# Kernel tuning notes

Hardware: AMD Instinct MI355X
Metric: run time of the kernel (lower is better)

The kernel has to match this reference:

```python
import jax, jax.numpy as jnp
import numpy as np

OLD_CL = 16
RATIO = 1.0
IGNORE_INDEX = 255


def setup_inputs() -> dict:
    key = jax.random.key(0)
    k1, k2 = jax.random.split(key)
    N, C, H, W = 8, 21, 512, 512
    inputs = jax.random.normal(k1, (N, C, H, W), dtype=jnp.float32)
    targets = jax.random.randint(k2, (N, H, W), 0, C).astype(jnp.int32)
    return {"inputs": inputs, "targets": targets}


def _forward(inputs, targets):
    N, C, H, W = inputs.shape
    # unbiased log-prob remap: old classes collapsed into channel 0
    den = jax.nn.logsumexp(inputs, axis=1)                       # [N,H,W]
    out0 = jax.nn.logsumexp(inputs[:, :OLD_CL], axis=1) - den    # [N,H,W]
    outputs = jnp.zeros_like(inputs)                             # channels 1..OLD_CL-1 stay 0
    outputs = outputs.at[:, 0].set(out0)
    outputs = outputs.at[:, OLD_CL:].set(inputs[:, OLD_CL:] - den[:, None])

    labels = jnp.where(targets < OLD_CL, 0, targets)             # [N,H,W]

    # per-sample class histogram (device-side replacement for the per-sample
    # cpu torch.histc loop). histc(bins=C, min=0, max=C-1) on integer-valued
    # labels counts occurrences per class, dropping values outside [0, C-1].
    lab_flat = labels.reshape(N, -1)
    in_range = lab_flat < C
    seg = jnp.where(in_range, lab_flat, 0) + jnp.arange(N, dtype=lab_flat.dtype)[:, None] * C
    hist = jax.ops.segment_sum(
        in_range.astype(jnp.float32).reshape(-1), seg.reshape(-1), num_segments=N * C
    ).reshape(N, C)

    cls = jnp.arange(C)
    idx_old = (cls < OLD_CL) & (cls != 0)                        # [C], old classes except 0
    idx0 = hist == 0                                             # computed on raw hist
    hist = hist.at[:, 0].set(hist[:, :OLD_CL].sum(axis=1))
    hist = jnp.where(idx_old[None, :], 0.0, hist)
    hist = jnp.where(idx0 & ~idx_old[None, :], 1.0, hist)
    weight = jnp.power(hist.sum(axis=1, keepdims=True) / hist, RATIO)
    weight = jnp.where(idx_old[None, :], 0.0, weight)            # kills the infs from /0
    weight = jax.lax.stop_gradient(weight)                       # torch .detach()

    outputs = outputs * weight[:, :, None, None]

    # nll_loss with ignore_index, mean reduction over valid pixels
    valid = labels != IGNORE_INDEX
    safe = jnp.where(valid, labels, 0)
    picked = jnp.take_along_axis(outputs, safe[:, None], axis=1)[:, 0]  # [N,H,W]
    vmask = valid.astype(outputs.dtype)
    return -(picked * vmask).sum() / vmask.sum()


def reference(inputs, targets):
    return _forward(inputs, targets)
```

## Files before the change

kernel.cpp:

```cpp
#include <hip/hip_runtime.h>

#define NS 8
#define NC 21
#define HW (512*512)
#define OLD 16
#define LBLK 128
#define LITER 2
#define PSTRIDE 16


__global__ void __launch_bounds__(256) loss_hist_kernel(const float* __restrict__ in,
                                                        const int* __restrict__ tgt,
                                                        float* __restrict__ part) {
    int n   = blockIdx.x >> 7;
    int blk = blockIdx.x & (LBLK - 1);
    const float* inN = in + (size_t)n * (NC * HW);
    const int4*  t4  = reinterpret_cast<const int4*>(tgt + (size_t)n * HW);

    float s[6]   = {0.f, 0.f, 0.f, 0.f, 0.f, 0.f};
    int   cnt[6] = {0, 0, 0, 0, 0, 0};

#pragma unroll 1
    for (int it = 0; it < LITER; ++it) {
        int g = (blk * LITER + it) * 256 + threadIdx.x;
        int p = g * 4;
        int4 t = t4[g];

        float4 sa  = make_float4(0.f, 0.f, 0.f, 0.f);
        float4 s16 = make_float4(0.f, 0.f, 0.f, 0.f);
        float4 xl  = make_float4(0.f, 0.f, 0.f, 0.f);

#pragma unroll
        for (int c = 0; c < NC; ++c) {
            float4 x = *reinterpret_cast<const float4*>(inN + (size_t)c * HW + p);
            sa.x += __expf(x.x);
            sa.y += __expf(x.y);
            sa.z += __expf(x.z);
            sa.w += __expf(x.w);
            if (c == OLD - 1) s16 = sa;
            if (c >= OLD) {
                xl.x = (t.x == c) ? x.x : xl.x;
                xl.y = (t.y == c) ? x.y : xl.y;
                xl.z = (t.z == c) ? x.z : xl.z;
                xl.w = (t.w == c) ? x.w : xl.w;
            }
        }

        int   labs[4] = {t.x, t.y, t.z, t.w};
        float sal[4]  = {sa.x, sa.y, sa.z, sa.w};
        float s16l[4] = {s16.x, s16.y, s16.z, s16.w};
        float xll[4]  = {xl.x, xl.y, xl.z, xl.w};
#pragma unroll
        for (int j = 0; j < 4; ++j) {
            int lab = labs[j] < OLD ? 0 : labs[j];
            float den = __logf(sal[j]);
            float val = (lab == 0 ? __logf(s16l[j]) : xll[j]) - den;

            bool h0 = (lab == 0);
            s[0]  += h0 ? val : 0.0f;  cnt[0] += h0;
#pragma unroll
            for (int k = 1; k < 6; ++k) {
                bool hk = (lab == 15 + k);
                s[k]  += hk ? val : 0.0f;
                cnt[k] += hk;
            }
        }
    }

#pragma unroll
    for (int off = 32; off > 0; off >>= 1)
#pragma unroll
        for (int k = 0; k < 6; ++k) {
            s[k]   += __shfl_down(s[k], off, 64);
            cnt[k] += __shfl_down(cnt[k], off, 64);
        }

    __shared__ float sp[4][6];
    __shared__ int   sc[4][6];
    int wave = threadIdx.x >> 6;
    if ((threadIdx.x & 63) == 0)
#pragma unroll
        for (int k = 0; k < 6; ++k) { sp[wave][k] = s[k]; sc[wave][k] = cnt[k]; }
    __syncthreads();
    if (threadIdx.x < 6) {
        int k = threadIdx.x;
        float fs = sp[0][k] + sp[1][k] + sp[2][k] + sp[3][k];
        int   ic = sc[0][k] + sc[1][k] + sc[2][k] + sc[3][k];
        part[(size_t)blockIdx.x * PSTRIDE + k] = fs;
        ((int*)part)[(size_t)blockIdx.x * PSTRIDE + 8 + k] = ic;
    }
}

__global__ void finalize_kernel(const float* __restrict__ part, float* __restrict__ out) {
    __shared__ double    ssum[NS][6];
    __shared__ int       shist[NS][6];
    __shared__ double    wsum[NS];
    __shared__ long long wcnt[NS];
    int t = threadIdx.x;

    if (t < NS * 12) {
        int n = t / 12, v = t % 12;
        if (v < 6) {
            double a = 0.0;
            for (int b = 0; b < LBLK; ++b)
                a += (double)part[(size_t)(n * LBLK + b) * PSTRIDE + v];
            ssum[n][v] = a;
        } else {
            int k = v - 6, a = 0;
            const int* ip = (const int*)part;
            for (int b = 0; b < LBLK; ++b)
                a += ip[(size_t)(n * LBLK + b) * PSTRIDE + 8 + k];
            shist[n][k] = a;
        }
    }
    __syncthreads();

    if (t < NS) {
        float h[6];
        float total = 0.0f;
        long long c = 0;
#pragma unroll
        for (int k = 0; k < 6; ++k) {
            int raw = shist[t][k];
            h[k] = (raw == 0) ? 1.0f : (float)raw;
            total += h[k];
            c += raw;
        }
        double acc = 0.0;
#pragma unroll
        for (int k = 0; k < 6; ++k)
            acc += (double)(total / h[k]) * ssum[t][k];
        wsum[t] = acc;
        wcnt[t] = c;
    }
    __syncthreads();

    if (t == 0) {
        double S = 0.0;
        long long C = 0;
        for (int n = 0; n < NS; ++n) { S += wsum[n]; C += wcnt[n]; }
        out[0] = (C > 0) ? (float)(-S / (double)C) : 0.0f;
    }
}

extern "C" void kernel_launch(void* const* d_in, const int* in_sizes, int n_in,
                              void* d_out, int out_size, void* d_ws, size_t ws_size,
                              hipStream_t stream) {
    const float* inputs  = (const float*)d_in[0];
    const int*   targets = (const int*)d_in[1];
    float*       out     = (float*)d_out;
    float*       part    = (float*)d_ws;

    loss_hist_kernel<<<NS * LBLK, 256, 0, stream>>>(inputs, targets, part);
    finalize_kernel<<<1, 128, 0, stream>>>(part, out);
}
```

Measured before the change: 251.4 us.

## Double loss-kernel grid to one tile per thread and parallelize finalize reduction

The main kernel now launches 2048 blocks, each thread handling a single 4-pixel group instead of looping twice, which raises the number of loads in flight. Partial sums move to a structure-of-arrays layout, and the finalize kernel reduces them with 512 threads and wave shuffles instead of serial per-thread loops over 128 blocks. The cost is twice as many partials and a float instead of double accumulation inside each wave.

```diff
diff --git a/kernel.cpp b/kernel.cpp
--- a/kernel.cpp
+++ b/kernel.cpp
@@ -4,66 +4,59 @@
 #define NC 21
 #define HW (512*512)
 #define OLD 16
-#define LBLK 128
-#define LITER 2
-#define PSTRIDE 16
+#define LBLK 256
+#define NBLK (NS * LBLK)
 
 
 __global__ void __launch_bounds__(256) loss_hist_kernel(const float* __restrict__ in,
                                                         const int* __restrict__ tgt,
                                                         float* __restrict__ part) {
-    int n   = blockIdx.x >> 7;
+    int n   = blockIdx.x >> 8;
     int blk = blockIdx.x & (LBLK - 1);
     const float* inN = in + (size_t)n * (NC * HW);
     const int4*  t4  = reinterpret_cast<const int4*>(tgt + (size_t)n * HW);
 
+    int g = blk * 256 + threadIdx.x;
+    int p = g * 4;
+    int4 t = t4[g];
+
+    float4 sa  = make_float4(0.f, 0.f, 0.f, 0.f);
+    float4 s16 = make_float4(0.f, 0.f, 0.f, 0.f);
+    float4 xl  = make_float4(0.f, 0.f, 0.f, 0.f);
+
+#pragma unroll
+    for (int c = 0; c < NC; ++c) {
+        float4 x = *reinterpret_cast<const float4*>(inN + (size_t)c * HW + p);
+        sa.x += __expf(x.x);
+        sa.y += __expf(x.y);
+        sa.z += __expf(x.z);
+        sa.w += __expf(x.w);
+        if (c == OLD - 1) s16 = sa;
+        if (c >= OLD) {
+            xl.x = (t.x == c) ? x.x : xl.x;
+            xl.y = (t.y == c) ? x.y : xl.y;
+            xl.z = (t.z == c) ? x.z : xl.z;
+            xl.w = (t.w == c) ? x.w : xl.w;
+        }
+    }
+
     float s[6]   = {0.f, 0.f, 0.f, 0.f, 0.f, 0.f};
     int   cnt[6] = {0, 0, 0, 0, 0, 0};
-
-#pragma unroll 1
-    for (int it = 0; it < LITER; ++it) {
-        int g = (blk * LITER + it) * 256 + threadIdx.x;
-        int p = g * 4;
-        int4 t = t4[g];
-
-        float4 sa  = make_float4(0.f, 0.f, 0.f, 0.f);
-        float4 s16 = make_float4(0.f, 0.f, 0.f, 0.f);
-        float4 xl  = make_float4(0.f, 0.f, 0.f, 0.f);
-
+    int   labs[4] = {t.x, t.y, t.z, t.w};
+    float sal[4]  = {sa.x, sa.y, sa.z, sa.w};
+    float s16l[4] = {s16.x, s16.y, s16.z, s16.w};
+    float xll[4]  = {xl.x, xl.y, xl.z, xl.w};
 #pragma unroll
-        for (int c = 0; c < NC; ++c) {
-            float4 x = *reinterpret_cast<const float4*>(inN + (size_t)c * HW + p);
-            sa.x += __expf(x.x);
-            sa.y += __expf(x.y);
-            sa.z += __expf(x.z);
-            sa.w += __expf(x.w);
-            if (c == OLD - 1) s16 = sa;
-            if (c >= OLD) {
-                xl.x = (t.x == c) ? x.x : xl.x;
-                xl.y = (t.y == c) ? x.y : xl.y;
-                xl.z = (t.z == c) ? x.z : xl.z;
-                xl.w = (t.w == c) ? x.w : xl.w;
-            }
-        }
-
-        int   labs[4] = {t.x, t.y, t.z, t.w};
-        float sal[4]  = {sa.x, sa.y, sa.z, sa.w};
-        float s16l[4] = {s16.x, s16.y, s16.z, s16.w};
-        float xll[4]  = {xl.x, xl.y, xl.z, xl.w};
+    for (int j = 0; j < 4; ++j) {
+        int lab = labs[j] < OLD ? 0 : labs[j];
+        float val = (lab == 0 ? __logf(s16l[j]) : xll[j]) - __logf(sal[j]);
+        bool h0 = (lab == 0);
+        s[0]  += h0 ? val : 0.0f;  cnt[0] += h0;
 #pragma unroll
-        for (int j = 0; j < 4; ++j) {
-            int lab = labs[j] < OLD ? 0 : labs[j];
-            float den = __logf(sal[j]);
-            float val = (lab == 0 ? __logf(s16l[j]) : xll[j]) - den;
-
-            bool h0 = (lab == 0);
-            s[0]  += h0 ? val : 0.0f;  cnt[0] += h0;
-#pragma unroll
-            for (int k = 1; k < 6; ++k) {
-                bool hk = (lab == 15 + k);
-                s[k]  += hk ? val : 0.0f;
-                cnt[k] += hk;
-            }
+        for (int k = 1; k < 6; ++k) {
+            bool hk = (lab == 15 + k);
+            s[k]  += hk ? val : 0.0f;
+            cnt[k] += hk;
         }
     }
 
@@ -84,61 +77,60 @@
     __syncthreads();
     if (threadIdx.x < 6) {
         int k = threadIdx.x;
-        float fs = sp[0][k] + sp[1][k] + sp[2][k] + sp[3][k];
-        int   ic = sc[0][k] + sc[1][k] + sc[2][k] + sc[3][k];
-        part[(size_t)blockIdx.x * PSTRIDE + k] = fs;
-        ((int*)part)[(size_t)blockIdx.x * PSTRIDE + 8 + k] = ic;
+        part[(size_t)k * NBLK + blockIdx.x] = sp[0][k] + sp[1][k] + sp[2][k] + sp[3][k];
+        ((int*)part)[(size_t)(6 + k) * NBLK + blockIdx.x] =
+            sc[0][k] + sc[1][k] + sc[2][k] + sc[3][k];
     }
 }
 
-__global__ void finalize_kernel(const float* __restrict__ part, float* __restrict__ out) {
+__global__ void __launch_bounds__(512) finalize_kernel(const float* __restrict__ part,
+                                                       float* __restrict__ out) {
+    int wave = threadIdx.x >> 6;
+    int lane = threadIdx.x & 63;
+    const int* ipart = (const int*)part;
+
+    float fs[6] = {0.f, 0.f, 0.f, 0.f, 0.f, 0.f};
+    int   ic[6] = {0, 0, 0, 0, 0, 0};
+#pragma unroll
+    for (int k = 0; k < 6; ++k)
+#pragma unroll
+        for (int c = 0; c < 4; ++c) {
+            int b = wave * LBLK + c * 64 + lane;
+            fs[k] += part[(size_t)k * NBLK + b];
+            ic[k] += ipart[(size_t)(6 + k) * NBLK + b];
+        }
+#pragma unroll
+    for (int off = 32; off > 0; off >>= 1)
+#pragma unroll
+        for (int k = 0; k < 6; ++k) {
+            fs[k] += __shfl_down(fs[k], off, 64);
+            ic[k] += __shfl_down(ic[k], off, 64);
+        }
+
     __shared__ double    ssum[NS][6];
     __shared__ int       shist[NS][6];
-    __shared__ double    wsum[NS];
-    __shared__ long long wcnt[NS];
-    int t = threadIdx.x;
-
-    if (t < NS * 12) {
-        int n = t / 12, v = t % 12;
-        if (v < 6) {
-            double a = 0.0;
-            for (int b = 0; b < LBLK; ++b)
-                a += (double)part[(size_t)(n * LBLK + b) * PSTRIDE + v];
-            ssum[n][v] = a;
-        } else {
-            int k = v - 6, a = 0;
-            const int* ip = (const int*)part;
-            for (int b = 0; b < LBLK; ++b)
-                a += ip[(size_t)(n * LBLK + b) * PSTRIDE + 8 + k];
-            shist[n][k] = a;
-        }
-    }
+    if (lane == 0)
+#pragma unroll
+        for (int k = 0; k < 6; ++k) { ssum[wave][k] = (double)fs[k]; shist[wave][k] = ic[k]; }
     __syncthreads();
 
-    if (t < NS) {
-        float h[6];
-        float total = 0.0f;
-        long long c = 0;
-#pragma unroll
-        for (int k = 0; k < 6; ++k) {
-            int raw = shist[t][k];
-            h[k] = (raw == 0) ? 1.0f : (float)raw;
-            total += h[k];
-            c += raw;
-        }
-        double acc = 0.0;
-#pragma unroll
-        for (int k = 0; k < 6; ++k)
-            acc += (double)(total / h[k]) * ssum[t][k];
-        wsum[t] = acc;
-        wcnt[t] = c;
-    }
-    __syncthreads();
-
-    if (t == 0) {
+    if (threadIdx.x == 0) {
         double S = 0.0;
         long long C = 0;
-        for (int n = 0; n < NS; ++n) { S += wsum[n]; C += wcnt[n]; }
+        for (int n = 0; n < NS; ++n) {
+            float h[6];
+            float total = 0.0f;
+#pragma unroll
+            for (int k = 0; k < 6; ++k) {
+                int raw = shist[n][k];
+                h[k] = (raw == 0) ? 1.0f : (float)raw;
+                total += h[k];
+                C += raw;
+            }
+#pragma unroll
+            for (int k = 0; k < 6; ++k)
+                S += (double)(total / h[k]) * ssum[n][k];
+        }
         out[0] = (C > 0) ? (float)(-S / (double)C) : 0.0f;
     }
 }
@@ -151,6 +143,6 @@
     float*       out     = (float*)d_out;
     float*       part    = (float*)d_ws;
 
-    loss_hist_kernel<<<NS * LBLK, 256, 0, stream>>>(inputs, targets, part);
-    finalize_kernel<<<1, 128, 0, stream>>>(part, out);
+    loss_hist_kernel<<<NBLK, 256, 0, stream>>>(inputs, targets, part);
+    finalize_kernel<<<1, 512, 0, stream>>>(part, out);
 }
```

Result: no change. 247.9 us (-1.4%).
